# Kernel optimization log

Hardware: AMD Instinct MI355X
Metric: run time of the kernel (lower is better)

## Reference

```python
import jax, jax.numpy as jnp
import numpy as np

N_ENS = 4        # number of FGL sub-layers
B, N_IN, N_OUT = 1, 16384, 4096
IN_C, OUT_C = 16, 16
DENSITY = 0.10   # sparsity proxy for A + dA random perturbation


def setup_inputs() -> dict:
    key = jax.random.key(0)
    kx, ka, km, kw, kb = jax.random.split(key, 5)
    x = jax.random.normal(kx, (B, N_IN, IN_C), dtype=jnp.float32)
    # Dense storage of the n perturbed sparse adjacencies A_i (n_out, n_in)
    A_vals = jax.random.normal(ka, (N_ENS, N_OUT, N_IN), dtype=jnp.float32)
    A_mask = jax.random.bernoulli(km, DENSITY, (N_ENS, N_OUT, N_IN))
    As = A_vals * A_mask.astype(jnp.float32)
    Ws = jax.random.normal(kw, (N_ENS, IN_C, OUT_C), dtype=jnp.float32) * (1.0 / np.sqrt(IN_C))
    bs = jax.random.normal(kb, (N_ENS, OUT_C), dtype=jnp.float32) * 0.01
    return {"x": x, "As": As, "Ws": Ws, "bs": bs}


def reference(x, As, Ws, bs):
    # Each FGL_i: y_i = (A_i @ x) @ W_i + b_i
    # x: [b, n_in, f]; As: [n, n_out, n_in]; Ws: [n, f, g]; bs: [n, g]
    h = jnp.einsum('noi,bif->nbof', As, x)            # graph aggregation per ensemble member
    y = jnp.einsum('nbof,nfg->nbog', h, Ws)           # per-member linear transform
    y = y + bs[:, None, None, :]
    return jnp.mean(y, axis=0)                        # sum over n members / n
```

## Files before the change

### kernel.cpp

```cpp
#include <hip/hip_runtime.h>


#define N_ENS 4
#define N_OUT 4096
#define N_IN  16384
#define ROWS  (N_ENS * N_OUT)
#define GSPLIT 32
#define ICHUNK (N_IN / GSPLIT)

__global__ __launch_bounds__(256, 4) void k_main(const float* __restrict__ A,
                                                 const float* __restrict__ x,
                                                 float* __restrict__ hp) {
    const int split  = blockIdx.x & (GSPLIT - 1);
    const int rowblk = blockIdx.x >> 5;
    const int tid    = threadIdx.x;
    const int row    = rowblk * 256 + tid;
    const int i0     = split * ICHUNK;

    __shared__ float xs[ICHUNK * 16];

    {
        const float4* xg = (const float4*)(x + (size_t)i0 * 16);
        float4* xl = (float4*)xs;
#pragma unroll
        for (int q = 0; q < 8; ++q)
            xl[tid + 256 * q] = xg[tid + 256 * q];
    }
    __syncthreads();

    const float* Ap = A + (size_t)row * N_IN + i0;

    float acc[16];
#pragma unroll
    for (int f = 0; f < 16; ++f) acc[f] = 0.0f;

#define COMPUTE(buf, sbase) do {                                         \
        const float* af_ = (const float*)(buf);                          \
        const float* xp_ = xs + (sbase) * 256;                           \
        _Pragma("unroll")                                                \
        for (int ii = 0; ii < 16; ++ii) {                                \
            const float av_ = af_[ii];                                   \
            _Pragma("unroll")                                            \
            for (int f = 0; f < 16; ++f)                                 \
                acc[f] = fmaf(av_, xp_[ii * 16 + f], acc[f]);            \
        }                                                                \
    } while (0)

    float4 aA[4], aB[4];
#pragma unroll
    for (int q = 0; q < 4; ++q) aA[q] = ((const float4*)Ap)[q];

    for (int s = 0; s < ICHUNK / 16; s += 2) {
#pragma unroll
        for (int q = 0; q < 4; ++q) aB[q] = ((const float4*)(Ap + (s + 1) * 16))[q];
        COMPUTE(aA, s);
        if (s + 2 < ICHUNK / 16) {
#pragma unroll
            for (int q = 0; q < 4; ++q) aA[q] = ((const float4*)(Ap + (s + 2) * 16))[q];
        }
        COMPUTE(aB, s + 1);
    }
#undef COMPUTE

    float* outp = hp + ((size_t)split * ROWS + row) * 16;
#pragma unroll
    for (int f = 0; f < 16; ++f) outp[f] = acc[f];
}

__global__ __launch_bounds__(256) void k_hsum(const float4* __restrict__ hp,
                                              float4* __restrict__ h) {
    int t = blockIdx.x * 256 + threadIdx.x;
    float4 s; s.x = 0.f; s.y = 0.f; s.z = 0.f; s.w = 0.f;
#pragma unroll
    for (int sp = 0; sp < GSPLIT; ++sp) {
        float4 v = hp[(size_t)sp * (ROWS * 4) + t];
        s.x += v.x; s.y += v.y; s.z += v.z; s.w += v.w;
    }
    h[t] = s;
}

__global__ __launch_bounds__(256) void k_out(const float* __restrict__ h,
                                             const float* __restrict__ Ws,
                                             const float* __restrict__ bs,
                                             float* __restrict__ out) {
    __shared__ float Wsm[N_ENS * 16 * 16];
    __shared__ float bsm[N_ENS * 16];
    int tid = threadIdx.x;
#pragma unroll
    for (int r = 0; r < 4; ++r) Wsm[tid + 256 * r] = Ws[tid + 256 * r];
    if (tid < 64) bsm[tid] = bs[tid];
    __syncthreads();

    int idx = blockIdx.x * 256 + tid;
    int o = idx >> 4;
    int gg = idx & 15;
    float s = 0.0f;
#pragma unroll
    for (int n = 0; n < N_ENS; ++n) {
        const float* hr = h + ((size_t)(n * N_OUT + o) << 4);
        float t = 0.0f;
#pragma unroll
        for (int f = 0; f < 16; ++f)
            t = fmaf(hr[f], Wsm[n * 256 + f * 16 + gg], t);
        s += t + bsm[n * 16 + gg];
    }
    out[idx] = 0.25f * s;
}

extern "C" void kernel_launch(void* const* d_in, const int* in_sizes, int n_in,
                              void* d_out, int out_size, void* d_ws, size_t ws_size,
                              hipStream_t stream) {
    const float* x  = (const float*)d_in[0];
    const float* As = (const float*)d_in[1];
    const float* Ws = (const float*)d_in[2];
    const float* bs = (const float*)d_in[3];
    float* out = (float*)d_out;

    float* hp = (float*)d_ws;
    float* h  = (float*)((char*)d_ws + (size_t)32 * 1024 * 1024);

    k_main<<<64 * GSPLIT, 256, 0, stream>>>(As, x, hp);
    k_hsum<<<(ROWS * 16 / 4) / 256, 256, 0, stream>>>((const float4*)hp, (float4*)h);
    k_out<<<(N_OUT * 16) / 256, 256, 0, stream>>>(h, Ws, bs, out);
}
```

Before: 1.420 ms.

## Stage A tiles through LDS for coalesced loads, read x directly from global

Each thread previously streamed its own A row with strided float4 loads, which coalesce poorly because each lane reads a different row. The kernel now loads 256x32 tiles of A cooperatively, with 8 lanes covering 128 contiguous bytes per row, and transposes them through padded LDS so each thread reads its row back. The x chunk is no longer staged in shared memory; it is read from global with wave-uniform addresses that should become scalar loads. This adds two barriers per stage and drops the occupancy hint, and puts x reads on the scalar or L1 cache path.

```diff
diff --git a/kernel.cpp b/kernel.cpp
--- a/kernel.cpp
+++ b/kernel.cpp
@@ -7,61 +7,63 @@
 #define ROWS  (N_ENS * N_OUT)
 #define GSPLIT 32
 #define ICHUNK (N_IN / GSPLIT)
+#define TI     32
+#define NSTAGE (ICHUNK / TI)
+#define LDP    36
 
-__global__ __launch_bounds__(256, 4) void k_main(const float* __restrict__ A,
-                                                 const float* __restrict__ x,
-                                                 float* __restrict__ hp) {
+__global__ __launch_bounds__(256) void k_main(const float* __restrict__ A,
+                                              const float* __restrict__ x,
+                                              float* __restrict__ hp) {
     const int split  = blockIdx.x & (GSPLIT - 1);
     const int rowblk = blockIdx.x >> 5;
     const int tid    = threadIdx.x;
-    const int row    = rowblk * 256 + tid;
     const int i0     = split * ICHUNK;
 
-    __shared__ float xs[ICHUNK * 16];
+    __shared__ float As_lds[256 * LDP];
 
-    {
-        const float4* xg = (const float4*)(x + (size_t)i0 * 16);
-        float4* xl = (float4*)xs;
-#pragma unroll
-        for (int q = 0; q < 8; ++q)
-            xl[tid + 256 * q] = xg[tid + 256 * q];
-    }
-    __syncthreads();
-
-    const float* Ap = A + (size_t)row * N_IN + i0;
+    const int srow = tid >> 3;
+    const int sq   = tid & 7;
+    const float* Ast = A + (size_t)(rowblk * 256 + srow) * N_IN + i0 + sq * 4;
 
     float acc[16];
 #pragma unroll
     for (int f = 0; f < 16; ++f) acc[f] = 0.0f;
 
-#define COMPUTE(buf, sbase) do {                                         \
-        const float* af_ = (const float*)(buf);                          \
-        const float* xp_ = xs + (sbase) * 256;                           \
-        _Pragma("unroll")                                                \
-        for (int ii = 0; ii < 16; ++ii) {                                \
-            const float av_ = af_[ii];                                   \
-            _Pragma("unroll")                                            \
-            for (int f = 0; f < 16; ++f)                                 \
-                acc[f] = fmaf(av_, xp_[ii * 16 + f], acc[f]);            \
-        }                                                                \
-    } while (0)
+    float4 pre[8];
+#pragma unroll
+    for (int p = 0; p < 8; ++p)
+        pre[p] = *(const float4*)(Ast + (size_t)(p * 32) * N_IN);
 
-    float4 aA[4], aB[4];
+    for (int s = 0; s < NSTAGE; ++s) {
+        __syncthreads();
 #pragma unroll
-    for (int q = 0; q < 4; ++q) aA[q] = ((const float4*)Ap)[q];
+        for (int p = 0; p < 8; ++p)
+            *(float4*)&As_lds[(p * 32 + srow) * LDP + sq * 4] = pre[p];
+        __syncthreads();
 
-    for (int s = 0; s < ICHUNK / 16; s += 2) {
+        if (s + 1 < NSTAGE) {
+            const float* An = Ast + (s + 1) * TI;
 #pragma unroll
-        for (int q = 0; q < 4; ++q) aB[q] = ((const float4*)(Ap + (s + 1) * 16))[q];
-        COMPUTE(aA, s);
-        if (s + 2 < ICHUNK / 16) {
+            for (int p = 0; p < 8; ++p)
+                pre[p] = *(const float4*)(An + (size_t)(p * 32) * N_IN);
+        }
+
+        const float* xp = x + ((size_t)i0 + s * TI) * 16;
+        float4 a4[8];
 #pragma unroll
-            for (int q = 0; q < 4; ++q) aA[q] = ((const float4*)(Ap + (s + 2) * 16))[q];
+        for (int q = 0; q < 8; ++q)
+            a4[q] = *(const float4*)&As_lds[tid * LDP + q * 4];
+        const float* af = (const float*)a4;
+#pragma unroll
+        for (int ii = 0; ii < TI; ++ii) {
+            const float av = af[ii];
+#pragma unroll
+            for (int f = 0; f < 16; ++f)
+                acc[f] = fmaf(av, xp[ii * 16 + f], acc[f]);
         }
-        COMPUTE(aB, s + 1);
     }
-#undef COMPUTE
 
+    const int row = rowblk * 256 + tid;
     float* outp = hp + ((size_t)split * ROWS + row) * 16;
 #pragma unroll
     for (int f = 0; f < 16; ++f) outp[f] = acc[f];
```

Result: slower. 1.554 ms (+9.4%).
